# Kernel tuning notes

Hardware: AMD Instinct MI355X
Metric: run time of the kernel (lower is better)

The kernel has to match this reference:

```python
import jax, jax.numpy as jnp
import numpy as np

N_NODES = 40000
N_EDGES = 640000
D_FEAT = 128


def setup_inputs() -> dict:
    key = jax.random.key(0)
    k1, k2, k3, k4 = jax.random.split(key, 4)
    x = jax.random.normal(k1, (N_NODES, D_FEAT), dtype=jnp.float32)
    beta = jax.random.uniform(k2, (1,), dtype=jnp.float32)
    # random edges guaranteed to have NO self-loops (module removes them anyway)
    row = jax.random.randint(k3, (N_EDGES,), 0, N_NODES)
    col = (row + 1 + jax.random.randint(k4, (N_EDGES,), 0, N_NODES - 1)) % N_NODES
    edge_index = jnp.stack([row, col]).astype(jnp.int64)
    return {"x": x, "beta": beta, "edge_index": edge_index}


def reference(x, beta, edge_index):
    num_nodes = x.shape[0]
    row, col = edge_index[0], edge_index[1]
    # add_self_loops (remove_self_loops is a no-op: inputs have none)
    loop = jnp.arange(num_nodes, dtype=row.dtype)
    row = jnp.concatenate([row, loop])  # [E+N]
    col = jnp.concatenate([col, loop])
    # per-edge cosine similarity scaled by beta
    norm = jnp.linalg.norm(x, axis=1)  # [N]
    alpha = jnp.sum(x[row] * x[col], axis=1) / (norm[row] * norm[col])  # [E+N]
    alpha = alpha * beta[0]
    # segment softmax grouped by destination node (row)
    amax = jax.ops.segment_max(alpha, row, num_segments=num_nodes)  # [N]
    alpha = jnp.exp(alpha - amax[row])
    denom = jax.ops.segment_sum(alpha, row, num_segments=num_nodes)  # [N]
    alpha = alpha / denom[row]
    # spmm: weighted scatter-aggregate of neighbor features
    out = jax.ops.segment_sum(alpha[:, None] * x[col], row, num_segments=num_nodes)  # [N, F]
    return out
```

## Files before the change

kernel.cpp:

```cpp
#include <hip/hip_runtime.h>
#include <math.h>

#define N_NODES 40000
#define N_EDGES 640000
#define D_FEAT 128
#define SLOTS 48
#define NGRP 8
#define MAXIT (SLOTS / NGRP)

__global__ void build_kernel(const int* __restrict__ row, const int* __restrict__ col,
                             int* __restrict__ count, int* __restrict__ ell) {
    int i = blockIdx.x * blockDim.x + threadIdx.x;
    if (i < N_EDGES) {
        int r = row[i];
        int rank = atomicAdd(&count[r], 1);
        if (rank < SLOTS) ell[r * SLOTS + rank] = col[i];
    }
}

__global__ __launch_bounds__(256)
void fused_kernel(const float* __restrict__ x, const float* __restrict__ beta,
                  const int* __restrict__ count, const int* __restrict__ ell,
                  float* __restrict__ out) {
    __shared__ float red[4][NGRP * D_FEAT];
    const int wid  = threadIdx.x >> 6;
    const int lane = threadIdx.x & 63;
    const int node = blockIdx.x * 4 + wid;
    const int g  = lane >> 3;
    const int hl = lane & 7;
    const int deg = min(count[node], SLOTS);
    const int NIT = (deg + NGRP - 1) >> 3;
    const int* eb = ell + node * SLOTS;

    int cidx[MAXIT];
    #pragma unroll
    for (int j = 0; j < MAXIT; j++) {
        int p = j * NGRP + g;
        cidx[j] = (p < deg) ? eb[p] : node;
    }

    const float* xrow = x + (size_t)node * D_FEAT;
    const float4* xn = (const float4*)xrow;
    float4 a0 = xn[hl], a1 = xn[8 + hl], a2 = xn[16 + hl], a3 = xn[24 + hl];
    float na2 = a0.x*a0.x + a0.y*a0.y + a0.z*a0.z + a0.w*a0.w
              + a1.x*a1.x + a1.y*a1.y + a1.z*a1.z + a1.w*a1.w
              + a2.x*a2.x + a2.y*a2.y + a2.z*a2.z + a2.w*a2.w
              + a3.x*a3.x + a3.y*a3.y + a3.z*a3.z + a3.w*a3.w;
    #pragma unroll
    for (int m = 1; m < NGRP; m <<= 1) na2 += __shfl_xor(na2, m);
    const float b0    = beta[0];
    const float scale = b0 * __frsqrt_rn(na2);
    const float selfw = __expf(b0);
    float4 acc0 = {0,0,0,0}, acc1 = {0,0,0,0}, acc2 = {0,0,0,0}, acc3 = {0,0,0,0};
    float den = 0.f;

    float4 A0, A1, A2, A3, B0, B1, B2, B3;
    {
        const float4* xc = (const float4*)(x + (size_t)cidx[0] * D_FEAT);
        A0 = xc[hl]; A1 = xc[8 + hl]; A2 = xc[16 + hl]; A3 = xc[24 + hl];
    }
    {
        const float4* xc = (const float4*)(x + (size_t)cidx[1] * D_FEAT);
        B0 = xc[hl]; B1 = xc[8 + hl]; B2 = xc[16 + hl]; B3 = xc[24 + hl];
    }

    #pragma unroll
    for (int j = 0; j < MAXIT; j++) {
        if (j >= NIT) break;
        float dot = a0.x*A0.x + a0.y*A0.y + a0.z*A0.z + a0.w*A0.w
                  + a1.x*A1.x + a1.y*A1.y + a1.z*A1.z + a1.w*A1.w
                  + a2.x*A2.x + a2.y*A2.y + a2.z*A2.z + a2.w*A2.w
                  + a3.x*A3.x + a3.y*A3.y + a3.z*A3.z + a3.w*A3.w;
        float nb2 = A0.x*A0.x + A0.y*A0.y + A0.z*A0.z + A0.w*A0.w
                  + A1.x*A1.x + A1.y*A1.y + A1.z*A1.z + A1.w*A1.w
                  + A2.x*A2.x + A2.y*A2.y + A2.z*A2.z + A2.w*A2.w
                  + A3.x*A3.x + A3.y*A3.y + A3.z*A3.z + A3.w*A3.w;
        #pragma unroll
        for (int m = 1; m < NGRP; m <<= 1) {
            dot += __shfl_xor(dot, m);
            nb2 += __shfl_xor(nb2, m);
        }
        float w = (j * NGRP + g < deg) ? __expf(dot * scale * __frsqrt_rn(nb2)) : 0.f;
        acc0.x += w*A0.x; acc0.y += w*A0.y; acc0.z += w*A0.z; acc0.w += w*A0.w;
        acc1.x += w*A1.x; acc1.y += w*A1.y; acc1.z += w*A1.z; acc1.w += w*A1.w;
        acc2.x += w*A2.x; acc2.y += w*A2.y; acc2.z += w*A2.z; acc2.w += w*A2.w;
        acc3.x += w*A3.x; acc3.y += w*A3.y; acc3.z += w*A3.z; acc3.w += w*A3.w;
        den += w;
        A0 = B0; A1 = B1; A2 = B2; A3 = B3;
        int cn = (j + 2 < MAXIT) ? cidx[j + 2] : node;
        const float4* xc = (const float4*)(x + (size_t)cn * D_FEAT);
        B0 = xc[hl]; B1 = xc[8 + hl]; B2 = xc[16 + hl]; B3 = xc[24 + hl];
    }

    {
        float4* rb4 = (float4*)red[wid];
        rb4[g*32 +      hl] = acc0;
        rb4[g*32 +  8 + hl] = acc1;
        rb4[g*32 + 16 + hl] = acc2;
        rb4[g*32 + 24 + hl] = acc3;
    }
    den += __shfl_xor(den, 8);
    den += __shfl_xor(den, 16);
    den += __shfl_xor(den, 32);
    __syncthreads();
    float sx = 0.f, sy = 0.f;
    #pragma unroll
    for (int q = 0; q < NGRP; q++) {
        float2 t = *(const float2*)&red[wid][q * D_FEAT + lane * 2];
        sx += t.x; sy += t.y;
    }
    float2 xs = ((const float2*)xrow)[lane];
    float inv = 1.0f / (den + selfw);
    float2 o = { (sx + selfw * xs.x) * inv, (sy + selfw * xs.y) * inv };
    ((float2*)(out + (size_t)node * D_FEAT))[lane] = o;
}

extern "C" void kernel_launch(void* const* d_in, const int* in_sizes, int n_in,
                              void* d_out, int out_size, void* d_ws, size_t ws_size,
                              hipStream_t stream) {
    const float* x    = (const float*)d_in[0];
    const float* beta = (const float*)d_in[1];
    const int*   row  = (const int*)d_in[2];
    const int*   col  = row + N_EDGES;
    float*       out  = (float*)d_out;

    int* count = (int*)d_ws;
    int* ell   = count + N_NODES;

    hipMemsetAsync(count, 0, N_NODES * sizeof(int), stream);

    build_kernel<<<(N_EDGES + 255) / 256, 256, 0, stream>>>(row, col, count, ell);

    fused_kernel<<<N_NODES / 4, 256, 0, stream>>>(x, beta, count, ell, out);
}
```

Measured before the change: 85.88 us.

## Process two nodes per wavefront and vectorize edge loads in ELL build

The fused kernel now maps two destination nodes to each 64-lane wavefront, each half-wave using 4 groups of 8 lanes, so each block covers 8 nodes. The loop runs to the max trip count of the two halves, and the block-wide __syncthreads before the shared-memory reduction is removed because each wave only reads its own region. The build kernel reads row and col as int4 and issues four atomics per thread. This aims to cut per-node wave underuse and sync cost for average degree around 16, but the pair of nodes in a wave now diverge in degree and each node gets fewer parallel gathers.

```diff
diff --git a/kernel.cpp b/kernel.cpp
--- a/kernel.cpp
+++ b/kernel.cpp
@@ -5,16 +5,20 @@
 #define N_EDGES 640000
 #define D_FEAT 128
 #define SLOTS 48
-#define NGRP 8
-#define MAXIT (SLOTS / NGRP)
+#define GPN 4
+#define MAXIT (SLOTS / GPN)
 
-__global__ void build_kernel(const int* __restrict__ row, const int* __restrict__ col,
+__global__ void build_kernel(const int4* __restrict__ rows4, const int4* __restrict__ cols4,
                              int* __restrict__ count, int* __restrict__ ell) {
     int i = blockIdx.x * blockDim.x + threadIdx.x;
-    if (i < N_EDGES) {
-        int r = row[i];
-        int rank = atomicAdd(&count[r], 1);
-        if (rank < SLOTS) ell[r * SLOTS + rank] = col[i];
+    if (i < N_EDGES / 4) {
+        int4 r4 = rows4[i];
+        int4 c4 = cols4[i];
+        int k;
+        k = atomicAdd(&count[r4.x], 1); if (k < SLOTS) ell[r4.x * SLOTS + k] = c4.x;
+        k = atomicAdd(&count[r4.y], 1); if (k < SLOTS) ell[r4.y * SLOTS + k] = c4.y;
+        k = atomicAdd(&count[r4.z], 1); if (k < SLOTS) ell[r4.z * SLOTS + k] = c4.z;
+        k = atomicAdd(&count[r4.w], 1); if (k < SLOTS) ell[r4.w * SLOTS + k] = c4.w;
     }
 }
 
@@ -22,20 +26,23 @@
 void fused_kernel(const float* __restrict__ x, const float* __restrict__ beta,
                   const int* __restrict__ count, const int* __restrict__ ell,
                   float* __restrict__ out) {
-    __shared__ float red[4][NGRP * D_FEAT];
+    __shared__ float red[4][2][GPN][132];
     const int wid  = threadIdx.x >> 6;
     const int lane = threadIdx.x & 63;
-    const int node = blockIdx.x * 4 + wid;
-    const int g  = lane >> 3;
-    const int hl = lane & 7;
-    const int deg = min(count[node], SLOTS);
-    const int NIT = (deg + NGRP - 1) >> 3;
+    const int h    = lane >> 5;
+    const int l32  = lane & 31;
+    const int g    = (lane >> 3) & 3;
+    const int hl   = lane & 7;
+    const int node = blockIdx.x * 8 + wid * 2 + h;
+    const int deg  = min(count[node], SLOTS);
+    const int NIT  = (deg + GPN - 1) >> 2;
+    int mx = max(NIT, __shfl_xor(NIT, 32));
     const int* eb = ell + node * SLOTS;
 
     int cidx[MAXIT];
     #pragma unroll
     for (int j = 0; j < MAXIT; j++) {
-        int p = j * NGRP + g;
+        int p = j * GPN + g;
         cidx[j] = (p < deg) ? eb[p] : node;
     }
 
@@ -47,7 +54,7 @@
               + a2.x*a2.x + a2.y*a2.y + a2.z*a2.z + a2.w*a2.w
               + a3.x*a3.x + a3.y*a3.y + a3.z*a3.z + a3.w*a3.w;
     #pragma unroll
-    for (int m = 1; m < NGRP; m <<= 1) na2 += __shfl_xor(na2, m);
+    for (int m = 1; m < 8; m <<= 1) na2 += __shfl_xor(na2, m);
     const float b0    = beta[0];
     const float scale = b0 * __frsqrt_rn(na2);
     const float selfw = __expf(b0);
@@ -66,7 +73,7 @@
 
     #pragma unroll
     for (int j = 0; j < MAXIT; j++) {
-        if (j >= NIT) break;
+        if (j >= mx) break;
         float dot = a0.x*A0.x + a0.y*A0.y + a0.z*A0.z + a0.w*A0.w
                   + a1.x*A1.x + a1.y*A1.y + a1.z*A1.z + a1.w*A1.w
                   + a2.x*A2.x + a2.y*A2.y + a2.z*A2.z + a2.w*A2.w
@@ -76,11 +83,11 @@
                   + A2.x*A2.x + A2.y*A2.y + A2.z*A2.z + A2.w*A2.w
                   + A3.x*A3.x + A3.y*A3.y + A3.z*A3.z + A3.w*A3.w;
         #pragma unroll
-        for (int m = 1; m < NGRP; m <<= 1) {
+        for (int m = 1; m < 8; m <<= 1) {
             dot += __shfl_xor(dot, m);
             nb2 += __shfl_xor(nb2, m);
         }
-        float w = (j * NGRP + g < deg) ? __expf(dot * scale * __frsqrt_rn(nb2)) : 0.f;
+        float w = (j * GPN + g < deg) ? __expf(dot * scale * __frsqrt_rn(nb2)) : 0.f;
         acc0.x += w*A0.x; acc0.y += w*A0.y; acc0.z += w*A0.z; acc0.w += w*A0.w;
         acc1.x += w*A1.x; acc1.y += w*A1.y; acc1.z += w*A1.z; acc1.w += w*A1.w;
         acc2.x += w*A2.x; acc2.y += w*A2.y; acc2.z += w*A2.z; acc2.w += w*A2.w;
@@ -92,27 +99,27 @@
         B0 = xc[hl]; B1 = xc[8 + hl]; B2 = xc[16 + hl]; B3 = xc[24 + hl];
     }
 
-    {
-        float4* rb4 = (float4*)red[wid];
-        rb4[g*32 +      hl] = acc0;
-        rb4[g*32 +  8 + hl] = acc1;
-        rb4[g*32 + 16 + hl] = acc2;
-        rb4[g*32 + 24 + hl] = acc3;
-    }
     den += __shfl_xor(den, 8);
     den += __shfl_xor(den, 16);
-    den += __shfl_xor(den, 32);
-    __syncthreads();
-    float sx = 0.f, sy = 0.f;
+
+    {
+        float4* rb = (float4*)red[wid][h][g];
+        rb[      hl] = acc0;
+        rb[ 8 + hl] = acc1;
+        rb[16 + hl] = acc2;
+        rb[24 + hl] = acc3;
+    }
+    float4 s = {0.f, 0.f, 0.f, 0.f};
     #pragma unroll
-    for (int q = 0; q < NGRP; q++) {
-        float2 t = *(const float2*)&red[wid][q * D_FEAT + lane * 2];
-        sx += t.x; sy += t.y;
+    for (int q = 0; q < GPN; q++) {
+        float4 t = ((const float4*)red[wid][h][q])[l32];
+        s.x += t.x; s.y += t.y; s.z += t.z; s.w += t.w;
     }
-    float2 xs = ((const float2*)xrow)[lane];
+    float4 xs = ((const float4*)xrow)[l32];
     float inv = 1.0f / (den + selfw);
-    float2 o = { (sx + selfw * xs.x) * inv, (sy + selfw * xs.y) * inv };
-    ((float2*)(out + (size_t)node * D_FEAT))[lane] = o;
+    float4 o = { (s.x + selfw * xs.x) * inv, (s.y + selfw * xs.y) * inv,
+                 (s.z + selfw * xs.z) * inv, (s.w + selfw * xs.w) * inv };
+    ((float4*)(out + (size_t)node * D_FEAT))[l32] = o;
 }
 
 extern "C" void kernel_launch(void* const* d_in, const int* in_sizes, int n_in,
@@ -129,7 +136,8 @@
 
     hipMemsetAsync(count, 0, N_NODES * sizeof(int), stream);
 
-    build_kernel<<<(N_EDGES + 255) / 256, 256, 0, stream>>>(row, col, count, ell);
+    build_kernel<<<(N_EDGES / 4 + 255) / 256, 256, 0, stream>>>(
+        (const int4*)row, (const int4*)col, count, ell);
 
-    fused_kernel<<<N_NODES / 4, 256, 0, stream>>>(x, beta, count, ell, out);
+    fused_kernel<<<N_NODES / 8, 256, 0, stream>>>(x, beta, count, ell, out);
 }
```

New measurement: 89.52 us. +4.2%, slower.
